# Kernel tuning notes

Hardware: AMD Instinct MI355X
Metric: run time of the kernel (lower is better)

## Reference

```python
import jax, jax.numpy as jnp
import numpy as np
import math

B, M, N = 1, 128, 256
LIG_C = 256      # rep_1d num_c
ATTN_C = 32      # attention_num_c
HEADS = 8        # num_heads
EPS = 1e-5


def setup_inputs() -> dict:
    key = jax.random.key(0)
    ks = jax.random.split(key, 8)
    s = 1.0 / math.sqrt(LIG_C)
    return {
        "lig_profile": jax.random.normal(ks[0], (B, M, N, LIG_C), dtype=jnp.float32),
        "ln_scale": jnp.ones((LIG_C,), dtype=jnp.float32),
        "ln_bias": jnp.zeros((LIG_C,), dtype=jnp.float32),
        "wq": jax.random.normal(ks[1], (LIG_C, ATTN_C * HEADS), dtype=jnp.float32) * s,
        "wk": jax.random.normal(ks[2], (LIG_C, ATTN_C * HEADS), dtype=jnp.float32) * s,
        "wv": jax.random.normal(ks[3], (LIG_C, ATTN_C * HEADS), dtype=jnp.float32) * s,
        "wf": jax.random.normal(ks[4], (ATTN_C * HEADS, LIG_C), dtype=jnp.float32) * s,
        "bf": jnp.zeros((LIG_C,), dtype=jnp.float32),
    }


def reference(lig_profile, ln_scale, ln_bias, wq, wk, wv, wf, bf):
    # LayerNorm over channel dim
    mu = jnp.mean(lig_profile, axis=-1, keepdims=True)
    var = jnp.mean(jnp.square(lig_profile - mu), axis=-1, keepdims=True)
    x = (lig_profile - mu) * jax.lax.rsqrt(var + EPS) * ln_scale + ln_bias

    # QKV projections; view splits last dim as (attn_c, heads) -> channel-major layout
    shape5 = x.shape[:-1] + (ATTN_C, HEADS)
    q = (x @ wq).reshape(shape5)  # [b,m,n,c,h]
    k = (x @ wk).reshape(shape5)
    v = (x @ wv).reshape(shape5)

    factor = 1.0 / math.sqrt(ATTN_C)
    aff = jnp.einsum('bmich,bmjch->bmijh', q, k) * factor  # [b,m,i,j,h]
    weights = jax.nn.softmax(aff, axis=-2)                  # softmax over j (keys)
    out = jnp.einsum('bmrch,bmirh->bmich', v, weights)      # [b,m,i,c,h]
    out = out.reshape(out.shape[:-2] + (ATTN_C * HEADS,))
    return out @ wf + bf
```

## Files before the change

kernel.cpp:

```cpp
#include <hip/hip_runtime.h>

typedef _Float16 f16;
typedef _Float16 f16x8 __attribute__((ext_vector_type(8)));
typedef _Float16 f16x4 __attribute__((ext_vector_type(4)));
typedef _Float16 f16x2 __attribute__((ext_vector_type(2)));
typedef float f32x4 __attribute__((ext_vector_type(4)));
typedef float f32x16 __attribute__((ext_vector_type(16)));

#define MDIM 128
#define NDIM 256
#define CDIM 256
#define ROWS (MDIM*NDIM)
#define L2E 1.4426950408889634f

__device__ inline int pk2(float a, float b) {
  union { f16x2 h; int i; } u;
  u.h[0] = (f16)a; u.h[1] = (f16)b;
  return u.i;
}

__global__ __launch_bounds__(256) void k_prep(
    const float* __restrict__ wq, const float* __restrict__ wk,
    const float* __restrict__ wv, const float* __restrict__ wf,
    f16* __restrict__ bq, f16* __restrict__ bk, f16* __restrict__ bv,
    f16* __restrict__ bw)
{
  __shared__ f16 ld[64][264];
  int which = blockIdx.x >> 2, kb = blockIdx.x & 3;
  int t = threadIdx.x;
  int k0 = kb * 64;
  if (which < 3) {
    const float* W = which == 0 ? wq : which == 1 ? wk : wv;
    f16* dst       = which == 0 ? bq : which == 1 ? bk : bv;
    float sc = which == 0 ? 0.17677669529663689f : 1.0f;
    for (int r = 0; r < 64; ++r)
      ld[r][t] = (f16)(W[(size_t)(k0 + r) * 256 + t] * sc);
    __syncthreads();
    int j = (t & 31) * 8 + (t >> 5);
#pragma unroll
    for (int rr = 0; rr < 8; ++rr) {
      f16x8 o;
#pragma unroll
      for (int i = 0; i < 8; ++i) o[i] = ld[rr * 8 + i][j];
      *(f16x8*)(dst + (size_t)t * 256 + k0 + rr * 8) = o;
    }
  } else {
    for (int r = 0; r < 64; ++r) {
      int ke = k0 + r;
      int jr = (ke & 31) * 8 + (ke >> 5);
      ld[r][t] = (f16)wf[(size_t)jr * 256 + t];
    }
    __syncthreads();
#pragma unroll
    for (int rr = 0; rr < 8; ++rr) {
      f16x8 o;
#pragma unroll
      for (int i = 0; i < 8; ++i) o[i] = ld[rr * 8 + i][t];
      *(f16x8*)(bw + (size_t)t * 256 + k0 + rr * 8) = o;
    }
  }
}

__global__ __launch_bounds__(256) void k_lnqkv(const float* __restrict__ x,
    const float* __restrict__ g, const float* __restrict__ bb,
    const f16* __restrict__ bq, const f16* __restrict__ bk, const f16* __restrict__ bv,
    f16* __restrict__ qo, f16* __restrict__ ko, f16* __restrict__ vT)
{
  __shared__ f16 As[64][264];
  __shared__ f16 Bs[64][264];
  __shared__ f16 vtmp[64][72];
  int bm = blockIdx.x;
  int t = threadIdx.x, lane = t & 63, w = t >> 6;
  int wr = w >> 1, wc = w & 1;
  int l15 = lane & 15, l4 = lane >> 4;
  int pr = t >> 2, pc = (t & 3) * 8;
  f16x8 pf[8];
#pragma unroll
  for (int p = 0; p < 8; ++p)
    pf[p] = *(const f16x8*)(bq + (size_t)pr * 256 + pc + p * 32);
  const float4 gv  = *(const float4*)(g + lane * 4);
  const float4 bv4 = *(const float4*)(bb + lane * 4);
#pragma unroll 4
  for (int rr = 0; rr < 16; ++rr) {
    int r = w * 16 + rr;
    const float4 xv = *(const float4*)(x + (size_t)(bm * 64 + r) * 256 + lane * 4);
    float s  = xv.x + xv.y + xv.z + xv.w;
    float s2 = xv.x*xv.x + xv.y*xv.y + xv.z*xv.z + xv.w*xv.w;
#pragma unroll
    for (int mm = 1; mm < 64; mm <<= 1) {
      s  += __shfl_xor(s,  mm, 64);
      s2 += __shfl_xor(s2, mm, 64);
    }
    float mu  = s * (1.0f / 256.0f);
    float var = s2 * (1.0f / 256.0f) - mu * mu;
    float rs  = rsqrtf(var + 1e-5f);
    f16x4 ov;
    ov[0] = (f16)((xv.x - mu) * rs * gv.x + bv4.x);
    ov[1] = (f16)((xv.y - mu) * rs * gv.y + bv4.y);
    ov[2] = (f16)((xv.z - mu) * rs * gv.z + bv4.z);
    ov[3] = (f16)((xv.w - mu) * rs * gv.w + bv4.w);
    *(f16x4*)&As[r][lane * 4] = ov;
  }
  for (int ct = 0; ct < 12; ++ct) {
    int je0 = (ct & 3) * 64;
#pragma unroll
    for (int p = 0; p < 8; ++p)
      *(f16x8*)&Bs[pr][pc + p * 32] = pf[p];
    __syncthreads();
    if (ct < 11) {
      const f16* Bn = (ct + 1) < 4 ? bq : (ct + 1) < 8 ? bk : bv;
      int je0n = ((ct + 1) & 3) * 64;
#pragma unroll
      for (int p = 0; p < 8; ++p)
        pf[p] = *(const f16x8*)(Bn + (size_t)(je0n + pr) * 256 + pc + p * 32);
    }
    f32x4 acc[2][2] = {};
#pragma unroll
    for (int kt = 0; kt < 8; ++kt) {
      f16x8 a0 = *(const f16x8*)&As[wr * 32 +      l15][kt * 32 + l4 * 8];
      f16x8 a1 = *(const f16x8*)&As[wr * 32 + 16 + l15][kt * 32 + l4 * 8];
      f16x8 b0 = *(const f16x8*)&Bs[wc * 32 +      l15][kt * 32 + l4 * 8];
      f16x8 b1 = *(const f16x8*)&Bs[wc * 32 + 16 + l15][kt * 32 + l4 * 8];
      acc[0][0] = __builtin_amdgcn_mfma_f32_16x16x32_f16(a0, b0, acc[0][0], 0, 0, 0);
      acc[0][1] = __builtin_amdgcn_mfma_f32_16x16x32_f16(a0, b1, acc[0][1], 0, 0, 0);
      acc[1][0] = __builtin_amdgcn_mfma_f32_16x16x32_f16(a1, b0, acc[1][0], 0, 0, 0);
      acc[1][1] = __builtin_amdgcn_mfma_f32_16x16x32_f16(a1, b1, acc[1][1], 0, 0, 0);
    }
    if (ct < 8) {
      f16* dst = ct < 4 ? qo : ko;
#pragma unroll
      for (int mi = 0; mi < 2; ++mi)
#pragma unroll
        for (int ni = 0; ni < 2; ++ni)
#pragma unroll
          for (int r = 0; r < 4; ++r) {
            int row = bm * 64 + wr * 32 + mi * 16 + l4 * 4 + r;
            int col = je0 + wc * 32 + ni * 16 + l15;
            dst[(size_t)row * 256 + col] = (f16)acc[mi][ni][r];
          }
    } else {
#pragma unroll
      for (int mi = 0; mi < 2; ++mi)
#pragma unroll
        for (int ni = 0; ni < 2; ++ni)
#pragma unroll
          for (int r = 0; r < 4; ++r)
            vtmp[wc * 32 + ni * 16 + l15][wr * 32 + mi * 16 + l4 * 4 + r] = (f16)acc[mi][ni][r];
      __syncthreads();
      int ch = t >> 2, np = (t & 3) * 16;
      size_t gdst = ((size_t)(bm >> 2) * 256 + je0 + ch) * 256 + (bm & 3) * 64 + np;
      *(f16x8*)(vT + gdst)     = *(const f16x8*)&vtmp[ch][np];
      *(f16x8*)(vT + gdst + 8) = *(const f16x8*)&vtmp[ch][np + 8];
    }
    __syncthreads();
  }
}

__global__ __launch_bounds__(512, 4) void k_attn(const f16* __restrict__ q,
    const f16* __restrict__ k, const f16* __restrict__ vT, f16* __restrict__ o)
{
  __shared__ f16 ks[256][40];
  __shared__ f16 vt[32][264];
  int bx = blockIdx.x;
  int m = bx >> 3, h = bx & 7;
  int t = threadIdx.x, lane = t & 63, w = t >> 6;
  int i32 = lane & 31, hi = lane >> 5;
  size_t rowbase = (size_t)m * 256;
#pragma unroll
  for (int p = 0; p < 2; ++p) {
    int n = p * 128 + (t >> 2);
    int c0 = (t & 3) * 8;
    *(f16x8*)&ks[n][c0] = *(const f16x8*)(k + (rowbase + n) * 256 + h * 32 + c0);
  }
#pragma unroll
  for (int p = 0; p < 2; ++p) {
    int idx = p * 512 + t;
    int c = idx >> 5, nb = (idx & 31) * 8;
    *(f16x8*)&vt[c][nb] = *(const f16x8*)(vT + ((size_t)m * 256 + h * 32 + c) * 256 + nb);
  }
  __syncthreads();
  int qi0 = w * 32;
  const f16* qp = q + (rowbase + qi0 + i32) * 256 + h * 32 + hi * 8;
  f16x8 qf0 = *(const f16x8*)(qp);
  f16x8 qf1 = *(const f16x8*)(qp + 16);
  f32x16 O = {};
  float m_run = -1e30f, l_run = 0.f;
#pragma unroll 2
  for (int kb = 0; kb < 8; ++kb) {
    f16x8 kf0 = *(const f16x8*)&ks[kb * 32 + i32][hi * 8];
    f16x8 kf1 = *(const f16x8*)&ks[kb * 32 + i32][16 + hi * 8];
    f32x16 s = {};
    __builtin_amdgcn_s_setprio(1);
    s = __builtin_amdgcn_mfma_f32_32x32x16_f16(kf0, qf0, s, 0, 0, 0);
    s = __builtin_amdgcn_mfma_f32_32x32x16_f16(kf1, qf1, s, 0, 0, 0);
    __builtin_amdgcn_s_setprio(0);
#pragma unroll
    for (int r = 0; r < 16; ++r) s[r] *= L2E;
    float pmax = s[0];
#pragma unroll
    for (int r = 1; r < 16; ++r) pmax = fmaxf(pmax, s[r]);
    pmax = fmaxf(pmax, __shfl_xor(pmax, 32, 64));
    if (!__all(pmax - m_run <= 8.f)) {
      float m_new = fmaxf(m_run, pmax);
      float f = __builtin_amdgcn_exp2f(m_run - m_new);
      l_run *= f;
#pragma unroll
      for (int r = 0; r < 16; ++r)
        O[r] *= __shfl(f, (r & 3) + 8 * (r >> 2) + 4 * hi, 64);
      m_run = m_new;
    }
    float lsum = 0.f;
#pragma unroll
    for (int r = 0; r < 16; ++r) {
      float e = __builtin_amdgcn_exp2f(s[r] - m_run);
      s[r] = e;
      lsum += e;
    }
    lsum += __shfl_xor(lsum, 32, 64);
    l_run += lsum;
    int W0[4], W1[4];
#pragma unroll
    for (int qq = 0; qq < 4; ++qq) {
      W0[qq] = pk2(s[4 * qq],     s[4 * qq + 1]);
      W1[qq] = pk2(s[4 * qq + 2], s[4 * qq + 3]);
    }
#pragma unroll
    for (int ks2 = 0; ks2 < 2; ++ks2) {
      int X0 = W0[2 * ks2], Y0 = W0[2 * ks2 + 1];
      int X1 = W1[2 * ks2], Y1 = W1[2 * ks2 + 1];
      int a0 = __shfl(X0, i32, 64),      b0 = __shfl(Y0, i32, 64);
      int a1 = __shfl(X1, i32, 64),      b1 = __shfl(Y1, i32, 64);
      int a2 = __shfl(X0, i32 + 32, 64), b2 = __shfl(Y0, i32 + 32, 64);
      int a3 = __shfl(X1, i32 + 32, 64), b3 = __shfl(Y1, i32 + 32, 64);
      union { unsigned int ww[4]; f16x8 v; } pa;
      pa.ww[0] = hi ? (unsigned)b0 : (unsigned)a0;
      pa.ww[1] = hi ? (unsigned)b1 : (unsigned)a1;
      pa.ww[2] = hi ? (unsigned)b2 : (unsigned)a2;
      pa.ww[3] = hi ? (unsigned)b3 : (unsigned)a3;
      f16x8 vb = *(const f16x8*)&vt[i32][kb * 32 + ks2 * 16 + hi * 8];
      __builtin_amdgcn_s_setprio(1);
      O = __builtin_amdgcn_mfma_f32_32x32x16_f16(pa.v, vb, O, 0, 0, 0);
      __builtin_amdgcn_s_setprio(0);
    }
  }
  float inv = 1.f / l_run;
#pragma unroll
  for (int r = 0; r < 16; ++r) {
    int i = (r & 3) + 8 * (r >> 2) + 4 * hi;
    float fr = __shfl(inv, i, 64);
    o[(rowbase + (size_t)(qi0 + i)) * 256 + h * 32 + i32] = (f16)(O[r] * fr);
  }
}

__global__ __launch_bounds__(256) void k_out(const f16* __restrict__ a,
    const f16* __restrict__ bw, const float* __restrict__ bias,
    float* __restrict__ out)
{
  __shared__ f16 As[64][264];
  __shared__ f16 Bs[64][264];
  int bm = blockIdx.x;
  int t = threadIdx.x, lane = t & 63, w = t >> 6;
  int wr = w >> 1, wc = w & 1;
  int l15 = lane & 15, l4 = lane >> 4;
  int pr = t >> 2, pc = (t & 3) * 8;
  f16x8 pf[8];
#pragma unroll
  for (int p = 0; p < 8; ++p)
    pf[p] = *(const f16x8*)(bw + (size_t)pr * 256 + pc + p * 32);
#pragma unroll
  for (int p = 0; p < 8; ++p)
    *(f16x8*)&As[pr][pc + p * 32] = *(const f16x8*)(a + (size_t)(bm * 64 + pr) * 256 + pc + p * 32);
  for (int ct = 0; ct < 4; ++ct) {
    int col0 = ct * 64;
#pragma unroll
    for (int p = 0; p < 8; ++p)
      *(f16x8*)&Bs[pr][pc + p * 32] = pf[p];
    __syncthreads();
    if (ct < 3) {
#pragma unroll
      for (int p = 0; p < 8; ++p)
        pf[p] = *(const f16x8*)(bw + (size_t)((ct + 1) * 64 + pr) * 256 + pc + p * 32);
    }
    f32x4 acc[2][2] = {};
#pragma unroll
    for (int kt = 0; kt < 8; ++kt) {
      f16x8 a0 = *(const f16x8*)&As[wr * 32 +      l15][kt * 32 + l4 * 8];
      f16x8 a1 = *(const f16x8*)&As[wr * 32 + 16 + l15][kt * 32 + l4 * 8];
      f16x8 b0 = *(const f16x8*)&Bs[wc * 32 +      l15][kt * 32 + l4 * 8];
      f16x8 b1 = *(const f16x8*)&Bs[wc * 32 + 16 + l15][kt * 32 + l4 * 8];
      acc[0][0] = __builtin_amdgcn_mfma_f32_16x16x32_f16(a0, b0, acc[0][0], 0, 0, 0);
      acc[0][1] = __builtin_amdgcn_mfma_f32_16x16x32_f16(a0, b1, acc[0][1], 0, 0, 0);
      acc[1][0] = __builtin_amdgcn_mfma_f32_16x16x32_f16(a1, b0, acc[1][0], 0, 0, 0);
      acc[1][1] = __builtin_amdgcn_mfma_f32_16x16x32_f16(a1, b1, acc[1][1], 0, 0, 0);
    }
#pragma unroll
    for (int mi = 0; mi < 2; ++mi)
#pragma unroll
      for (int ni = 0; ni < 2; ++ni)
#pragma unroll
        for (int r = 0; r < 4; ++r) {
          int row = bm * 64 + wr * 32 + mi * 16 + l4 * 4 + r;
          int col = col0 + wc * 32 + ni * 16 + l15;
          out[(size_t)row * 256 + col] = acc[mi][ni][r] + bias[col];
        }
    __syncthreads();
  }
}

extern "C" void kernel_launch(void* const* d_in, const int* in_sizes, int n_in,
                              void* d_out, int out_size, void* d_ws, size_t ws_size,
                              hipStream_t stream)
{
  const float* x  = (const float*)d_in[0];
  const float* g  = (const float*)d_in[1];
  const float* b  = (const float*)d_in[2];
  const float* wq = (const float*)d_in[3];
  const float* wk = (const float*)d_in[4];
  const float* wv = (const float*)d_in[5];
  const float* wf = (const float*)d_in[6];
  const float* bf = (const float*)d_in[7];
  float* out = (float*)d_out;

  char* ws = (char*)d_ws;
  f16* ah  = (f16*)(ws);
  f16* qh  = (f16*)(ws + (size_t)16 * 1024 * 1024);
  f16* kh  = (f16*)(ws + (size_t)32 * 1024 * 1024);
  f16* vTh = (f16*)(ws + (size_t)48 * 1024 * 1024);
  char* wbase = ws + (size_t)64 * 1024 * 1024;
  f16* bq = (f16*)(wbase);
  f16* bk = (f16*)(wbase + 128 * 1024);
  f16* bv = (f16*)(wbase + 256 * 1024);
  f16* bw = (f16*)(wbase + 384 * 1024);

  k_prep <<<16,   256, 0, stream>>>(wq, wk, wv, wf, bq, bk, bv, bw);
  k_lnqkv<<<512,  256, 0, stream>>>(x, g, b, bq, bk, bv, qh, kh, vTh);
  k_attn <<<1024, 512, 0, stream>>>(qh, kh, vTh, ah);
  k_out  <<<512,  256, 0, stream>>>(ah, bw, bf, out);
}
```

Baseline: 82.23 us.

## Read weight fragments directly from global memory in QKV and output GEMMs

The QKV projection and output projection kernels no longer stage weight tiles in shared memory with a per-column-tile loop and barriers. Each of 8 waves now owns a strip of output columns, reads its B fragments straight from global (L2-cached) memory, and reuses one shared A tile across 4 row sub-tiles. The V transpose goes through a per-wave scratch buffer, so no block-wide sync is needed. This cuts LDS traffic and barriers, but every wave issues its own uncoalesced-ish global weight loads, relying on cache hits.

```diff
diff --git a/kernel.cpp b/kernel.cpp
--- a/kernel.cpp
+++ b/kernel.cpp
@@ -61,28 +61,21 @@
   }
 }
 
-__global__ __launch_bounds__(256) void k_lnqkv(const float* __restrict__ x,
+__global__ __launch_bounds__(512) void k_lnqkv(const float* __restrict__ x,
     const float* __restrict__ g, const float* __restrict__ bb,
     const f16* __restrict__ bq, const f16* __restrict__ bk, const f16* __restrict__ bv,
     f16* __restrict__ qo, f16* __restrict__ ko, f16* __restrict__ vT)
 {
   __shared__ f16 As[64][264];
-  __shared__ f16 Bs[64][264];
-  __shared__ f16 vtmp[64][72];
+  __shared__ f16 vtmp[8][16][72];
   int bm = blockIdx.x;
   int t = threadIdx.x, lane = t & 63, w = t >> 6;
-  int wr = w >> 1, wc = w & 1;
   int l15 = lane & 15, l4 = lane >> 4;
-  int pr = t >> 2, pc = (t & 3) * 8;
-  f16x8 pf[8];
-#pragma unroll
-  for (int p = 0; p < 8; ++p)
-    pf[p] = *(const f16x8*)(bq + (size_t)pr * 256 + pc + p * 32);
   const float4 gv  = *(const float4*)(g + lane * 4);
   const float4 bv4 = *(const float4*)(bb + lane * 4);
-#pragma unroll 4
-  for (int rr = 0; rr < 16; ++rr) {
-    int r = w * 16 + rr;
+#pragma unroll
+  for (int rr = 0; rr < 8; ++rr) {
+    int r = w * 8 + rr;
     const float4 xv = *(const float4*)(x + (size_t)(bm * 64 + r) * 256 + lane * 4);
     float s  = xv.x + xv.y + xv.z + xv.w;
     float s2 = xv.x*xv.x + xv.y*xv.y + xv.z*xv.z + xv.w*xv.w;
@@ -101,58 +94,51 @@
     ov[3] = (f16)((xv.w - mu) * rs * gv.w + bv4.w);
     *(f16x4*)&As[r][lane * 4] = ov;
   }
-  for (int ct = 0; ct < 12; ++ct) {
-    int je0 = (ct & 3) * 64;
-#pragma unroll
-    for (int p = 0; p < 8; ++p)
-      *(f16x8*)&Bs[pr][pc + p * 32] = pf[p];
-    __syncthreads();
-    if (ct < 11) {
-      const f16* Bn = (ct + 1) < 4 ? bq : (ct + 1) < 8 ? bk : bv;
-      int je0n = ((ct + 1) & 3) * 64;
-#pragma unroll
-      for (int p = 0; p < 8; ++p)
-        pf[p] = *(const f16x8*)(Bn + (size_t)(je0n + pr) * 256 + pc + p * 32);
-    }
-    f32x4 acc[2][2] = {};
+  __syncthreads();
+  for (int it = 0; it < 2; ++it) {
+    int gc0 = it * 384 + w * 48;
+    f32x4 acc[4][3] = {};
 #pragma unroll
     for (int kt = 0; kt < 8; ++kt) {
-      f16x8 a0 = *(const f16x8*)&As[wr * 32 +      l15][kt * 32 + l4 * 8];
-      f16x8 a1 = *(const f16x8*)&As[wr * 32 + 16 + l15][kt * 32 + l4 * 8];
-      f16x8 b0 = *(const f16x8*)&Bs[wc * 32 +      l15][kt * 32 + l4 * 8];
-      f16x8 b1 = *(const f16x8*)&Bs[wc * 32 + 16 + l15][kt * 32 + l4 * 8];
-      acc[0][0] = __builtin_amdgcn_mfma_f32_16x16x32_f16(a0, b0, acc[0][0], 0, 0, 0);
-      acc[0][1] = __builtin_amdgcn_mfma_f32_16x16x32_f16(a0, b1, acc[0][1], 0, 0, 0);
-      acc[1][0] = __builtin_amdgcn_mfma_f32_16x16x32_f16(a1, b0, acc[1][0], 0, 0, 0);
-      acc[1][1] = __builtin_amdgcn_mfma_f32_16x16x32_f16(a1, b1, acc[1][1], 0, 0, 0);
-    }
-    if (ct < 8) {
-      f16* dst = ct < 4 ? qo : ko;
-#pragma unroll
-      for (int mi = 0; mi < 2; ++mi)
-#pragma unroll
-        for (int ni = 0; ni < 2; ++ni)
-#pragma unroll
-          for (int r = 0; r < 4; ++r) {
-            int row = bm * 64 + wr * 32 + mi * 16 + l4 * 4 + r;
-            int col = je0 + wc * 32 + ni * 16 + l15;
-            dst[(size_t)row * 256 + col] = (f16)acc[mi][ni][r];
-          }
-    } else {
-#pragma unroll
-      for (int mi = 0; mi < 2; ++mi)
-#pragma unroll
-        for (int ni = 0; ni < 2; ++ni)
+      f16x8 af[4];
+#pragma unroll
+      for (int mi = 0; mi < 4; ++mi)
+        af[mi] = *(const f16x8*)&As[mi * 16 + l15][kt * 32 + l4 * 8];
+#pragma unroll
+      for (int ni = 0; ni < 3; ++ni) {
+        int gc = gc0 + ni * 16;
+        const f16* B = gc < 256 ? bq : gc < 512 ? bk : bv;
+        f16x8 bf = *(const f16x8*)(B + (size_t)((gc & 255) + l15) * 256 + kt * 32 + l4 * 8);
+#pragma unroll
+        for (int mi = 0; mi < 4; ++mi)
+          acc[mi][ni] = __builtin_amdgcn_mfma_f32_16x16x32_f16(af[mi], bf, acc[mi][ni], 0, 0, 0);
+      }
+    }
+#pragma unroll
+    for (int ni = 0; ni < 3; ++ni) {
+      int gc = gc0 + ni * 16;
+      if (gc < 512) {
+        f16* dst = gc < 256 ? qo : ko;
+        int col = (gc & 255) + l15;
+#pragma unroll
+        for (int mi = 0; mi < 4; ++mi)
 #pragma unroll
           for (int r = 0; r < 4; ++r)
-            vtmp[wc * 32 + ni * 16 + l15][wr * 32 + mi * 16 + l4 * 4 + r] = (f16)acc[mi][ni][r];
-      __syncthreads();
-      int ch = t >> 2, np = (t & 3) * 16;
-      size_t gdst = ((size_t)(bm >> 2) * 256 + je0 + ch) * 256 + (bm & 3) * 64 + np;
-      *(f16x8*)(vT + gdst)     = *(const f16x8*)&vtmp[ch][np];
-      *(f16x8*)(vT + gdst + 8) = *(const f16x8*)&vtmp[ch][np + 8];
-    }
-    __syncthreads();
+            dst[(size_t)(bm * 64 + mi * 16 + l4 * 4 + r) * 256 + col] = (f16)acc[mi][ni][r];
+      } else {
+#pragma unroll
+        for (int mi = 0; mi < 4; ++mi)
+#pragma unroll
+          for (int r = 0; r < 4; ++r)
+            vtmp[w][l15][mi * 16 + l4 * 4 + r] = (f16)acc[mi][ni][r];
+        int ch = lane >> 2, nq = (lane & 3) * 16;
+        f16x8 v0 = *(const f16x8*)&vtmp[w][ch][nq];
+        f16x8 v1 = *(const f16x8*)&vtmp[w][ch][nq + 8];
+        size_t gdst = ((size_t)(bm >> 2) * 256 + (gc & 255) + ch) * 256 + (bm & 3) * 64 + nq;
+        *(f16x8*)(vT + gdst)     = v0;
+        *(f16x8*)(vT + gdst + 8) = v1;
+      }
+    }
   }
 }
 
@@ -252,59 +238,46 @@
   }
 }
 
-__global__ __launch_bounds__(256) void k_out(const f16* __restrict__ a,
+__global__ __launch_bounds__(512) void k_out(const f16* __restrict__ a,
     const f16* __restrict__ bw, const float* __restrict__ bias,
     float* __restrict__ out)
 {
   __shared__ f16 As[64][264];
-  __shared__ f16 Bs[64][264];
   int bm = blockIdx.x;
   int t = threadIdx.x, lane = t & 63, w = t >> 6;
-  int wr = w >> 1, wc = w & 1;
   int l15 = lane & 15, l4 = lane >> 4;
-  int pr = t >> 2, pc = (t & 3) * 8;
-  f16x8 pf[8];
-#pragma unroll
-  for (int p = 0; p < 8; ++p)
-    pf[p] = *(const f16x8*)(bw + (size_t)pr * 256 + pc + p * 32);
-#pragma unroll
-  for (int p = 0; p < 8; ++p)
-    *(f16x8*)&As[pr][pc + p * 32] = *(const f16x8*)(a + (size_t)(bm * 64 + pr) * 256 + pc + p * 32);
-  for (int ct = 0; ct < 4; ++ct) {
-    int col0 = ct * 64;
-#pragma unroll
-    for (int p = 0; p < 8; ++p)
-      *(f16x8*)&Bs[pr][pc + p * 32] = pf[p];
-    __syncthreads();
-    if (ct < 3) {
-#pragma unroll
-      for (int p = 0; p < 8; ++p)
-        pf[p] = *(const f16x8*)(bw + (size_t)((ct + 1) * 64 + pr) * 256 + pc + p * 32);
-    }
-    f32x4 acc[2][2] = {};
-#pragma unroll
-    for (int kt = 0; kt < 8; ++kt) {
-      f16x8 a0 = *(const f16x8*)&As[wr * 32 +      l15][kt * 32 + l4 * 8];
-      f16x8 a1 = *(const f16x8*)&As[wr * 32 + 16 + l15][kt * 32 + l4 * 8];
-      f16x8 b0 = *(const f16x8*)&Bs[wc * 32 +      l15][kt * 32 + l4 * 8];
-      f16x8 b1 = *(const f16x8*)&Bs[wc * 32 + 16 + l15][kt * 32 + l4 * 8];
-      acc[0][0] = __builtin_amdgcn_mfma_f32_16x16x32_f16(a0, b0, acc[0][0], 0, 0, 0);
-      acc[0][1] = __builtin_amdgcn_mfma_f32_16x16x32_f16(a0, b1, acc[0][1], 0, 0, 0);
-      acc[1][0] = __builtin_amdgcn_mfma_f32_16x16x32_f16(a1, b0, acc[1][0], 0, 0, 0);
-      acc[1][1] = __builtin_amdgcn_mfma_f32_16x16x32_f16(a1, b1, acc[1][1], 0, 0, 0);
-    }
-#pragma unroll
-    for (int mi = 0; mi < 2; ++mi)
-#pragma unroll
-      for (int ni = 0; ni < 2; ++ni)
-#pragma unroll
-        for (int r = 0; r < 4; ++r) {
-          int row = bm * 64 + wr * 32 + mi * 16 + l4 * 4 + r;
-          int col = col0 + wc * 32 + ni * 16 + l15;
-          out[(size_t)row * 256 + col] = acc[mi][ni][r] + bias[col];
-        }
-    __syncthreads();
-  }
+#pragma unroll
+  for (int p = 0; p < 4; ++p) {
+    int idx = p * 512 + t;
+    int r = idx >> 5, c0 = (idx & 31) * 8;
+    *(f16x8*)&As[r][c0] = *(const f16x8*)(a + (size_t)(bm * 64 + r) * 256 + c0);
+  }
+  __syncthreads();
+  int gc0 = w * 32;
+  f32x4 acc[4][2] = {};
+#pragma unroll
+  for (int kt = 0; kt < 8; ++kt) {
+    f16x8 af[4];
+#pragma unroll
+    for (int mi = 0; mi < 4; ++mi)
+      af[mi] = *(const f16x8*)&As[mi * 16 + l15][kt * 32 + l4 * 8];
+#pragma unroll
+    for (int ni = 0; ni < 2; ++ni) {
+      f16x8 bf = *(const f16x8*)(bw + (size_t)(gc0 + ni * 16 + l15) * 256 + kt * 32 + l4 * 8);
+#pragma unroll
+      for (int mi = 0; mi < 4; ++mi)
+        acc[mi][ni] = __builtin_amdgcn_mfma_f32_16x16x32_f16(af[mi], bf, acc[mi][ni], 0, 0, 0);
+    }
+  }
+  float b0 = bias[gc0 + l15], b1 = bias[gc0 + 16 + l15];
+#pragma unroll
+  for (int mi = 0; mi < 4; ++mi)
+#pragma unroll
+    for (int r = 0; r < 4; ++r) {
+      int row = bm * 64 + mi * 16 + l4 * 4 + r;
+      out[(size_t)row * 256 + gc0 + l15]      = acc[mi][0][r] + b0;
+      out[(size_t)row * 256 + gc0 + 16 + l15] = acc[mi][1][r] + b1;
+    }
 }
 
 extern "C" void kernel_launch(void* const* d_in, const int* in_sizes, int n_in,
@@ -333,7 +306,7 @@
   f16* bw = (f16*)(wbase + 384 * 1024);
 
   k_prep <<<16,   256, 0, stream>>>(wq, wk, wv, wf, bq, bk, bv, bw);
-  k_lnqkv<<<512,  256, 0, stream>>>(x, g, b, bq, bk, bv, qh, kh, vTh);
+  k_lnqkv<<<512,  512, 0, stream>>>(x, g, b, bq, bk, bv, qh, kh, vTh);
   k_attn <<<1024, 512, 0, stream>>>(qh, kh, vTh, ah);
-  k_out  <<<512,  256, 0, stream>>>(ah, bw, bf, out);
-}
+  k_out  <<<512,  512, 0, stream>>>(ah, bw, bf, out);
+}
```

Result: slower. 95.14 us (+15.7%).

## Fuse attention with output projection and split weight prep across more blocks

Applied to the files above, without the earlier changes.

Merges the attention and output-projection kernels into one. Each block handles 64 query rows of one m, loops over all 8 heads, and accumulates the normalized attention output straight into 8 f32x16 accumulators against the f16 output weights read from global memory. This removes the f16 attention-output round trip through HBM and one kernel launch. The MFMA operand order is swapped so the per-row rescale needs no shuffle. The weight-prep kernel is also split into 64 blocks instead of 16 for more parallelism. In exchange, blocks use 128 threads with a heavy accumulator register load, grid parallelism drops, and K/V are reloaded per head with serial syncs.

```diff
diff --git a/kernel.cpp b/kernel.cpp
--- a/kernel.cpp
+++ b/kernel.cpp
@@ -25,39 +25,41 @@
     f16* __restrict__ bq, f16* __restrict__ bk, f16* __restrict__ bv,
     f16* __restrict__ bw)
 {
-  __shared__ f16 ld[64][264];
-  int which = blockIdx.x >> 2, kb = blockIdx.x & 3;
+  __shared__ f16 ld[16][264];
+  int which = blockIdx.x >> 4, kb = blockIdx.x & 15;
   int t = threadIdx.x;
-  int k0 = kb * 64;
+  int k0 = kb * 16;
   if (which < 3) {
     const float* W = which == 0 ? wq : which == 1 ? wk : wv;
     f16* dst       = which == 0 ? bq : which == 1 ? bk : bv;
     float sc = which == 0 ? 0.17677669529663689f : 1.0f;
-    for (int r = 0; r < 64; ++r)
+#pragma unroll
+    for (int r = 0; r < 16; ++r)
       ld[r][t] = (f16)(W[(size_t)(k0 + r) * 256 + t] * sc);
     __syncthreads();
     int j = (t & 31) * 8 + (t >> 5);
-#pragma unroll
-    for (int rr = 0; rr < 8; ++rr) {
-      f16x8 o;
-#pragma unroll
-      for (int i = 0; i < 8; ++i) o[i] = ld[rr * 8 + i][j];
-      *(f16x8*)(dst + (size_t)t * 256 + k0 + rr * 8) = o;
-    }
+    f16x8 o;
+#pragma unroll
+    for (int i = 0; i < 8; ++i) o[i] = ld[i][j];
+    *(f16x8*)(dst + (size_t)t * 256 + k0) = o;
+#pragma unroll
+    for (int i = 0; i < 8; ++i) o[i] = ld[8 + i][j];
+    *(f16x8*)(dst + (size_t)t * 256 + k0 + 8) = o;
   } else {
-    for (int r = 0; r < 64; ++r) {
+#pragma unroll
+    for (int r = 0; r < 16; ++r) {
       int ke = k0 + r;
       int jr = (ke & 31) * 8 + (ke >> 5);
       ld[r][t] = (f16)wf[(size_t)jr * 256 + t];
     }
     __syncthreads();
-#pragma unroll
-    for (int rr = 0; rr < 8; ++rr) {
-      f16x8 o;
-#pragma unroll
-      for (int i = 0; i < 8; ++i) o[i] = ld[rr * 8 + i][t];
-      *(f16x8*)(bw + (size_t)t * 256 + k0 + rr * 8) = o;
-    }
+    f16x8 o;
+#pragma unroll
+    for (int i = 0; i < 8; ++i) o[i] = ld[i][t];
+    *(f16x8*)(bw + (size_t)t * 256 + k0) = o;
+#pragma unroll
+    for (int i = 0; i < 8; ++i) o[i] = ld[8 + i][t];
+    *(f16x8*)(bw + (size_t)t * 256 + k0 + 8) = o;
   }
 }
 
@@ -156,73 +158,103 @@
   }
 }
 
-__global__ __launch_bounds__(512, 4) void k_attn(const f16* __restrict__ q,
-    const f16* __restrict__ k, const f16* __restrict__ vT, f16* __restrict__ o)
+__global__ __launch_bounds__(128) void k_attnout(const f16* __restrict__ q,
+    const f16* __restrict__ k, const f16* __restrict__ vT,
+    const f16* __restrict__ bw, const float* __restrict__ bias,
+    float* __restrict__ out)
 {
-  __shared__ f16 ks[256][40];
+  __shared__ f16 ksh[256][40];
   __shared__ f16 vt[32][264];
   int bx = blockIdx.x;
-  int m = bx >> 3, h = bx & 7;
+  int m = bx >> 2, qq = bx & 3;
   int t = threadIdx.x, lane = t & 63, w = t >> 6;
   int i32 = lane & 31, hi = lane >> 5;
   size_t rowbase = (size_t)m * 256;
-#pragma unroll
-  for (int p = 0; p < 2; ++p) {
-    int n = p * 128 + (t >> 2);
-    int c0 = (t & 3) * 8;
-    *(f16x8*)&ks[n][c0] = *(const f16x8*)(k + (rowbase + n) * 256 + h * 32 + c0);
-  }
-#pragma unroll
-  for (int p = 0; p < 2; ++p) {
-    int idx = p * 512 + t;
-    int c = idx >> 5, nb = (idx & 31) * 8;
-    *(f16x8*)&vt[c][nb] = *(const f16x8*)(vT + ((size_t)m * 256 + h * 32 + c) * 256 + nb);
-  }
-  __syncthreads();
-  int qi0 = w * 32;
-  const f16* qp = q + (rowbase + qi0 + i32) * 256 + h * 32 + hi * 8;
-  f16x8 qf0 = *(const f16x8*)(qp);
-  f16x8 qf1 = *(const f16x8*)(qp + 16);
-  f32x16 O = {};
-  float m_run = -1e30f, l_run = 0.f;
+  int qi0 = qq * 64 + w * 32;
+  f32x16 oa[8] = {};
+  for (int h = 0; h < 8; ++h) {
+    __syncthreads();
+#pragma unroll
+    for (int p = 0; p < 8; ++p) {
+      int n = p * 32 + (t >> 2);
+      int c0 = (t & 3) * 8;
+      *(f16x8*)&ksh[n][c0] = *(const f16x8*)(k + (rowbase + n) * 256 + h * 32 + c0);
+    }
+#pragma unroll
+    for (int p = 0; p < 8; ++p) {
+      int idx = p * 128 + t;
+      int c = idx >> 5, nb = (idx & 31) * 8;
+      *(f16x8*)&vt[c][nb] = *(const f16x8*)(vT + ((size_t)m * 256 + h * 32 + c) * 256 + nb);
+    }
+    __syncthreads();
+    const f16* qp = q + (rowbase + qi0 + i32) * 256 + h * 32 + hi * 8;
+    f16x8 qf0 = *(const f16x8*)(qp);
+    f16x8 qf1 = *(const f16x8*)(qp + 16);
+    f32x16 O = {};
+    float m_run = -1e30f, l_run = 0.f;
 #pragma unroll 2
-  for (int kb = 0; kb < 8; ++kb) {
-    f16x8 kf0 = *(const f16x8*)&ks[kb * 32 + i32][hi * 8];
-    f16x8 kf1 = *(const f16x8*)&ks[kb * 32 + i32][16 + hi * 8];
-    f32x16 s = {};
-    __builtin_amdgcn_s_setprio(1);
-    s = __builtin_amdgcn_mfma_f32_32x32x16_f16(kf0, qf0, s, 0, 0, 0);
-    s = __builtin_amdgcn_mfma_f32_32x32x16_f16(kf1, qf1, s, 0, 0, 0);
-    __builtin_amdgcn_s_setprio(0);
-#pragma unroll
-    for (int r = 0; r < 16; ++r) s[r] *= L2E;
-    float pmax = s[0];
-#pragma unroll
-    for (int r = 1; r < 16; ++r) pmax = fmaxf(pmax, s[r]);
-    pmax = fmaxf(pmax, __shfl_xor(pmax, 32, 64));
-    if (!__all(pmax - m_run <= 8.f)) {
-      float m_new = fmaxf(m_run, pmax);
-      float f = __builtin_amdgcn_exp2f(m_run - m_new);
-      l_run *= f;
-#pragma unroll
-      for (int r = 0; r < 16; ++r)
-        O[r] *= __shfl(f, (r & 3) + 8 * (r >> 2) + 4 * hi, 64);
-      m_run = m_new;
-    }
-    float lsum = 0.f;
-#pragma unroll
-    for (int r = 0; r < 16; ++r) {
-      float e = __builtin_amdgcn_exp2f(s[r] - m_run);
-      s[r] = e;
-      lsum += e;
-    }
-    lsum += __shfl_xor(lsum, 32, 64);
-    l_run += lsum;
+    for (int kb = 0; kb < 8; ++kb) {
+      f16x8 kf0 = *(const f16x8*)&ksh[kb * 32 + i32][hi * 8];
+      f16x8 kf1 = *(const f16x8*)&ksh[kb * 32 + i32][16 + hi * 8];
+      f32x16 s = {};
+      __builtin_amdgcn_s_setprio(1);
+      s = __builtin_amdgcn_mfma_f32_32x32x16_f16(kf0, qf0, s, 0, 0, 0);
+      s = __builtin_amdgcn_mfma_f32_32x32x16_f16(kf1, qf1, s, 0, 0, 0);
+      __builtin_amdgcn_s_setprio(0);
+#pragma unroll
+      for (int r = 0; r < 16; ++r) s[r] *= L2E;
+      float pmax = s[0];
+#pragma unroll
+      for (int r = 1; r < 16; ++r) pmax = fmaxf(pmax, s[r]);
+      pmax = fmaxf(pmax, __shfl_xor(pmax, 32, 64));
+      if (!__all(pmax - m_run <= 8.f)) {
+        float m_new = fmaxf(m_run, pmax);
+        float f = __builtin_amdgcn_exp2f(m_run - m_new);
+        l_run *= f;
+#pragma unroll
+        for (int r = 0; r < 16; ++r) O[r] *= f;
+        m_run = m_new;
+      }
+      float lsum = 0.f;
+#pragma unroll
+      for (int r = 0; r < 16; ++r) {
+        float e = __builtin_amdgcn_exp2f(s[r] - m_run);
+        s[r] = e;
+        lsum += e;
+      }
+      lsum += __shfl_xor(lsum, 32, 64);
+      l_run += lsum;
+      int W0[4], W1[4];
+#pragma unroll
+      for (int qn = 0; qn < 4; ++qn) {
+        W0[qn] = pk2(s[4 * qn],     s[4 * qn + 1]);
+        W1[qn] = pk2(s[4 * qn + 2], s[4 * qn + 3]);
+      }
+#pragma unroll
+      for (int ks2 = 0; ks2 < 2; ++ks2) {
+        int X0 = W0[2 * ks2], Y0 = W0[2 * ks2 + 1];
+        int X1 = W1[2 * ks2], Y1 = W1[2 * ks2 + 1];
+        int a0 = __shfl(X0, i32, 64),      b0 = __shfl(Y0, i32, 64);
+        int a1 = __shfl(X1, i32, 64),      b1 = __shfl(Y1, i32, 64);
+        int a2 = __shfl(X0, i32 + 32, 64), b2 = __shfl(Y0, i32 + 32, 64);
+        int a3 = __shfl(X1, i32 + 32, 64), b3 = __shfl(Y1, i32 + 32, 64);
+        union { unsigned int ww[4]; f16x8 v; } pa;
+        pa.ww[0] = hi ? (unsigned)b0 : (unsigned)a0;
+        pa.ww[1] = hi ? (unsigned)b1 : (unsigned)a1;
+        pa.ww[2] = hi ? (unsigned)b2 : (unsigned)a2;
+        pa.ww[3] = hi ? (unsigned)b3 : (unsigned)a3;
+        f16x8 vb = *(const f16x8*)&vt[i32][kb * 32 + ks2 * 16 + hi * 8];
+        __builtin_amdgcn_s_setprio(1);
+        O = __builtin_amdgcn_mfma_f32_32x32x16_f16(vb, pa.v, O, 0, 0, 0);
+        __builtin_amdgcn_s_setprio(0);
+      }
+    }
+    float inv = 1.f / l_run;
     int W0[4], W1[4];
 #pragma unroll
-    for (int qq = 0; qq < 4; ++qq) {
-      W0[qq] = pk2(s[4 * qq],     s[4 * qq + 1]);
-      W1[qq] = pk2(s[4 * qq + 2], s[4 * qq + 3]);
+    for (int qn = 0; qn < 4; ++qn) {
+      W0[qn] = pk2(O[4 * qn] * inv,     O[4 * qn + 1] * inv);
+      W1[qn] = pk2(O[4 * qn + 2] * inv, O[4 * qn + 3] * inv);
     }
 #pragma unroll
     for (int ks2 = 0; ks2 < 2; ++ks2) {
@@ -232,78 +264,26 @@
       int a1 = __shfl(X1, i32, 64),      b1 = __shfl(Y1, i32, 64);
       int a2 = __shfl(X0, i32 + 32, 64), b2 = __shfl(Y0, i32 + 32, 64);
       int a3 = __shfl(X1, i32 + 32, 64), b3 = __shfl(Y1, i32 + 32, 64);
-      union { unsigned int ww[4]; f16x8 v; } pa;
-      pa.ww[0] = hi ? (unsigned)b0 : (unsigned)a0;
-      pa.ww[1] = hi ? (unsigned)b1 : (unsigned)a1;
-      pa.ww[2] = hi ? (unsigned)b2 : (unsigned)a2;
-      pa.ww[3] = hi ? (unsigned)b3 : (unsigned)a3;
-      f16x8 vb = *(const f16x8*)&vt[i32][kb * 32 + ks2 * 16 + hi * 8];
-      __builtin_amdgcn_s_setprio(1);
-      O = __builtin_amdgcn_mfma_f32_32x32x16_f16(pa.v, vb, O, 0, 0, 0);
-      __builtin_amdgcn_s_setprio(0);
-    }
-  }
-  float inv = 1.f / l_run;
-#pragma unroll
-  for (int r = 0; r < 16; ++r) {
-    int i = (r & 3) + 8 * (r >> 2) + 4 * hi;
-    float fr = __shfl(inv, i, 64);
-    o[(rowbase + (size_t)(qi0 + i)) * 256 + h * 32 + i32] = (f16)(O[r] * fr);
-  }
-}
-
-__global__ __launch_bounds__(256) void k_out(const f16* __restrict__ a,
-    const f16* __restrict__ bw, const float* __restrict__ bias,
-    float* __restrict__ out)
-{
-  __shared__ f16 As[64][264];
-  __shared__ f16 Bs[64][264];
-  int bm = blockIdx.x;
-  int t = threadIdx.x, lane = t & 63, w = t >> 6;
-  int wr = w >> 1, wc = w & 1;
-  int l15 = lane & 15, l4 = lane >> 4;
-  int pr = t >> 2, pc = (t & 3) * 8;
-  f16x8 pf[8];
-#pragma unroll
-  for (int p = 0; p < 8; ++p)
-    pf[p] = *(const f16x8*)(bw + (size_t)pr * 256 + pc + p * 32);
-#pragma unroll
-  for (int p = 0; p < 8; ++p)
-    *(f16x8*)&As[pr][pc + p * 32] = *(const f16x8*)(a + (size_t)(bm * 64 + pr) * 256 + pc + p * 32);
-  for (int ct = 0; ct < 4; ++ct) {
-    int col0 = ct * 64;
-#pragma unroll
-    for (int p = 0; p < 8; ++p)
-      *(f16x8*)&Bs[pr][pc + p * 32] = pf[p];
-    __syncthreads();
-    if (ct < 3) {
-#pragma unroll
-      for (int p = 0; p < 8; ++p)
-        pf[p] = *(const f16x8*)(bw + (size_t)((ct + 1) * 64 + pr) * 256 + pc + p * 32);
-    }
-    f32x4 acc[2][2] = {};
-#pragma unroll
-    for (int kt = 0; kt < 8; ++kt) {
-      f16x8 a0 = *(const f16x8*)&As[wr * 32 +      l15][kt * 32 + l4 * 8];
-      f16x8 a1 = *(const f16x8*)&As[wr * 32 + 16 + l15][kt * 32 + l4 * 8];
-      f16x8 b0 = *(const f16x8*)&Bs[wc * 32 +      l15][kt * 32 + l4 * 8];
-      f16x8 b1 = *(const f16x8*)&Bs[wc * 32 + 16 + l15][kt * 32 + l4 * 8];
-      acc[0][0] = __builtin_amdgcn_mfma_f32_16x16x32_f16(a0, b0, acc[0][0], 0, 0, 0);
-      acc[0][1] = __builtin_amdgcn_mfma_f32_16x16x32_f16(a0, b1, acc[0][1], 0, 0, 0);
-      acc[1][0] = __builtin_amdgcn_mfma_f32_16x16x32_f16(a1, b0, acc[1][0], 0, 0, 0);
-      acc[1][1] = __builtin_amdgcn_mfma_f32_16x16x32_f16(a1, b1, acc[1][1], 0, 0, 0);
-    }
-#pragma unroll
-    for (int mi = 0; mi < 2; ++mi)
-#pragma unroll
-      for (int ni = 0; ni < 2; ++ni)
-#pragma unroll
-        for (int r = 0; r < 4; ++r) {
-          int row = bm * 64 + wr * 32 + mi * 16 + l4 * 4 + r;
-          int col = col0 + wc * 32 + ni * 16 + l15;
-          out[(size_t)row * 256 + col] = acc[mi][ni][r] + bias[col];
-        }
-    __syncthreads();
+      union { unsigned int ww[4]; f16x8 v; } of;
+      of.ww[0] = hi ? (unsigned)b0 : (unsigned)a0;
+      of.ww[1] = hi ? (unsigned)b1 : (unsigned)a1;
+      of.ww[2] = hi ? (unsigned)b2 : (unsigned)a2;
+      of.ww[3] = hi ? (unsigned)b3 : (unsigned)a3;
+#pragma unroll
+      for (int cf = 0; cf < 8; ++cf) {
+        f16x8 bf = *(const f16x8*)(bw + (size_t)(cf * 32 + i32) * 256 + h * 32 + ks2 * 16 + hi * 8);
+        oa[cf] = __builtin_amdgcn_mfma_f32_32x32x16_f16(of.v, bf, oa[cf], 0, 0, 0);
+      }
+    }
+  }
+#pragma unroll
+  for (int cf = 0; cf < 8; ++cf) {
+    float bv = bias[cf * 32 + i32];
+#pragma unroll
+    for (int r = 0; r < 16; ++r) {
+      int qrow = (r & 3) + 8 * (r >> 2) + 4 * hi;
+      out[(rowbase + (size_t)(qi0 + qrow)) * 256 + cf * 32 + i32] = oa[cf][r] + bv;
+    }
   }
 }
 
@@ -322,7 +302,6 @@
   float* out = (float*)d_out;
 
   char* ws = (char*)d_ws;
-  f16* ah  = (f16*)(ws);
   f16* qh  = (f16*)(ws + (size_t)16 * 1024 * 1024);
   f16* kh  = (f16*)(ws + (size_t)32 * 1024 * 1024);
   f16* vTh = (f16*)(ws + (size_t)48 * 1024 * 1024);
@@ -332,8 +311,7 @@
   f16* bv = (f16*)(wbase + 256 * 1024);
   f16* bw = (f16*)(wbase + 384 * 1024);
 
-  k_prep <<<16,   256, 0, stream>>>(wq, wk, wv, wf, bq, bk, bv, bw);
-  k_lnqkv<<<512,  256, 0, stream>>>(x, g, b, bq, bk, bv, qh, kh, vTh);
-  k_attn <<<1024, 512, 0, stream>>>(qh, kh, vTh, ah);
-  k_out  <<<512,  256, 0, stream>>>(ah, bw, bf, out);
-}
+  k_prep   <<<64,   256, 0, stream>>>(wq, wk, wv, wf, bq, bk, bv, bw);
+  k_lnqkv  <<<512,  256, 0, stream>>>(x, g, b, bq, bk, bv, qh, kh, vTh);
+  k_attnout<<<512,  128, 0, stream>>>(qh, kh, vTh, bw, bf, out);
+}
```

Result: slower. 144.3 us (+75.4%).
